# Kernel tuning notes

Hardware: AMD Instinct MI355X
Metric: run time of the kernel (lower is better)

The kernel has to match this reference:

```python
import jax, jax.numpy as jnp
import numpy as np

B, G, D, H, KD = 32, 512, 128, 4, 32  # batch, graph, embed_dim, n_heads, key_dim=embed//heads
NORM = 1.0 / np.sqrt(KD).astype(np.float32)  # MultiHeadCompat norm_factor = 1/sqrt(key_dim)


def _uniform(k, shape, fan):
    s = 1.0 / np.sqrt(fan).astype(np.float32)
    return jax.random.uniform(k, shape, jnp.float32, -s, s)


def setup_inputs() -> dict:
    key = jax.random.key(0)
    ks = jax.random.split(key, 16)
    inp = {
        "h": jax.random.normal(ks[0], (B, G, D), jnp.float32),
        "pos_pickup": jax.random.randint(ks[1], (B,), 0, G),
        "pos_delivery": jax.random.randint(ks[2], (B,), 0, G),
        "rec": jax.random.randint(ks[3], (B, G), 0, G),
        # compater_insert1 / compater_insert2 projections: (n_heads, input_dim, key_dim)
        "Wq1": _uniform(ks[4], (H, D, KD), KD),
        "Wk1": _uniform(ks[5], (H, D, KD), KD),
        "Wq2": _uniform(ks[6], (H, D, KD), KD),
        "Wk2": _uniform(ks[7], (H, D, KD), KD),
        # agg MLP(16, 32, 32, 1); stored as (in, out) so y = x @ W + b
        "fc1_w": _uniform(ks[8], (16, 32), 16),
        "fc1_b": _uniform(ks[9], (32,), 32),
        "fc2_w": _uniform(ks[10], (32, 32), 32),
        "fc2_b": _uniform(ks[11], (32,), 32),
        "fc3_w": _uniform(ks[12], (32, 1), 32),
        "fc3_b": _uniform(ks[13], (1,), 1),
    }
    return inp


def _compat(qv, hh, Wq, Wk):
    # qv: (B, D) single query node; hh: (B, G, D)
    Q = jnp.einsum('bd,hdk->bhk', qv, Wq)       # (B, H, K)
    K = jnp.einsum('bgd,hdk->bhgk', hh, Wk)     # (B, H, G, K)
    return NORM * jnp.einsum('bhk,bhgk->bgh', Q, K)  # (B, G, H)


def reference(h, pos_pickup, pos_delivery, rec, Wq1, Wk1, Wq2, Wk2,
              fc1_w, fc1_b, fc2_w, fc2_b, fc3_w, fc3_b):
    b, g, d = h.shape
    ar = jnp.arange(b)
    h_pickup = h[ar, pos_pickup]      # (B, D)
    h_delivery = h[ar, pos_delivery]  # (B, D)
    h_neighbour = jnp.take_along_axis(h, rec[:, :, None], axis=1)  # (B, G, D)

    shp = (b, g, g, 4)
    c_pp = jnp.broadcast_to(_compat(h_pickup, h, Wq1, Wk1)[:, :, None, :], shp)
    c_po = jnp.broadcast_to(_compat(h_pickup, h_neighbour, Wq2, Wk2)[:, :, None, :], shp)
    c_dp = jnp.broadcast_to(_compat(h_delivery, h, Wq1, Wk1)[:, None, :, :], shp)
    c_do = jnp.broadcast_to(_compat(h_delivery, h_neighbour, Wq2, Wk2)[:, None, :, :], shp)
    x = jnp.concatenate([c_pp, c_po, c_dp, c_do], axis=-1)  # (B, G, G, 16)

    # agg MLP (dropout p=0.05 is identity at inference)
    x = jax.nn.relu(x @ fc1_w + fc1_b)
    x = jax.nn.relu(x @ fc2_w + fc2_b)
    return (x @ fc3_w + fc3_b)[..., 0]  # (B, G, G)
```

## Files before the change

### kernel.cpp

```cpp
#include <hip/hip_runtime.h>


#define B 32
#define G 512
#define D 128
#define NH 4
#define KD 32
#define NORMF 0.17677669529663687f

#define WS_APQ 0
#define WS_APO 16384
#define WS_ADP 32768
#define WS_ADO 49152
#define WS_P   65536
#define WS_Q   589824

typedef float v16f __attribute__((ext_vector_type(16)));
typedef _Float16 v8h __attribute__((ext_vector_type(8)));
typedef __fp16 v2fp __attribute__((ext_vector_type(2)));

union H8 { v8h v; v2fp h2[4]; };

__global__ __launch_bounds__(128) void precompute_A(
    const float* __restrict__ h, const int* __restrict__ pp, const int* __restrict__ pd,
    const float* __restrict__ Wq1, const float* __restrict__ Wk1,
    const float* __restrict__ Wq2, const float* __restrict__ Wk2,
    float* __restrict__ ws) {
  const int b = blockIdx.x;
  const int t = threadIdx.x;
  __shared__ float hp[D], hd[D];
  __shared__ float q1p[NH * KD], q2p[NH * KD], q1d[NH * KD], q2d[NH * KD];

  hp[t] = h[(b * G + pp[b]) * D + t];
  hd[t] = h[(b * G + pd[b]) * D + t];
  __syncthreads();

  {
    const int hh = t >> 5, k = t & 31;
    const float* wq1 = Wq1 + hh * D * KD + k;
    const float* wq2 = Wq2 + hh * D * KD + k;
    float s1p = 0.f, s2p = 0.f, s1d = 0.f, s2d = 0.f;
    for (int d = 0; d < D; ++d) {
      const float w1 = wq1[d * KD], w2 = wq2[d * KD];
      const float xp = hp[d], xd = hd[d];
      s1p = fmaf(xp, w1, s1p);
      s2p = fmaf(xp, w2, s2p);
      s1d = fmaf(xd, w1, s1d);
      s2d = fmaf(xd, w2, s2d);
    }
    q1p[t] = s1p; q2p[t] = s2p; q1d[t] = s1d; q2d[t] = s2d;
  }
  __syncthreads();

  const int d = t;
  for (int hh = 0; hh < NH; ++hh) {
    const float* wk1 = Wk1 + hh * D * KD + d * KD;
    const float* wk2 = Wk2 + hh * D * KD + d * KD;
    float apq = 0.f, apo = 0.f, adp = 0.f, ado = 0.f;
#pragma unroll
    for (int k = 0; k < KD; ++k) {
      const float w1 = wk1[k], w2 = wk2[k];
      apq = fmaf(q1p[hh * 32 + k], w1, apq);
      adp = fmaf(q1d[hh * 32 + k], w1, adp);
      apo = fmaf(q2p[hh * 32 + k], w2, apo);
      ado = fmaf(q2d[hh * 32 + k], w2, ado);
    }
    const int o = b * (NH * D) + hh * D + d;
    ws[WS_APQ + o] = NORMF * apq;
    ws[WS_APO + o] = NORMF * apo;
    ws[WS_ADP + o] = NORMF * adp;
    ws[WS_ADO + o] = NORMF * ado;
  }
}

__global__ __launch_bounds__(256) void compute_PQ(
    const float* __restrict__ h, const int* __restrict__ rec,
    const float* __restrict__ fc1_w, const float* __restrict__ fc1_b,
    float* __restrict__ ws) {
  const int bx = blockIdx.x;
  const int b = bx >> 3, g0 = (bx & 7) * 64;
  const int t = threadIdx.x;
  const int gl = t & 63;
  const int hh = __builtin_amdgcn_readfirstlane(t >> 6);
  const int g = g0 + gl;

  __shared__ float sc[64][17];
  __shared__ float sout[64][33];

  const float* Apq = ws + WS_APQ + (b * NH + hh) * D;
  const float* Apo = ws + WS_APO + (b * NH + hh) * D;
  const float* Adp = ws + WS_ADP + (b * NH + hh) * D;
  const float* Ado = ws + WS_ADO + (b * NH + hh) * D;
  const float4* hg4 = (const float4*)(h + ((size_t)b * G + g) * D);
  const float4* hn4 = (const float4*)(h + ((size_t)b * G + rec[b * G + g]) * D);

  float cpp = 0.f, cpo = 0.f, cdp = 0.f, cdo = 0.f;
#pragma unroll 4
  for (int d4 = 0; d4 < 32; ++d4) {
    const float4 x = hg4[d4], y = hn4[d4];
    const float4 a1 = *(const float4*)(Apq + d4 * 4);
    const float4 a2 = *(const float4*)(Apo + d4 * 4);
    const float4 a3 = *(const float4*)(Adp + d4 * 4);
    const float4 a4 = *(const float4*)(Ado + d4 * 4);
    cpp = fmaf(x.x, a1.x, fmaf(x.y, a1.y, fmaf(x.z, a1.z, fmaf(x.w, a1.w, cpp))));
    cpo = fmaf(y.x, a2.x, fmaf(y.y, a2.y, fmaf(y.z, a2.z, fmaf(y.w, a2.w, cpo))));
    cdp = fmaf(x.x, a3.x, fmaf(x.y, a3.y, fmaf(x.z, a3.z, fmaf(x.w, a3.w, cdp))));
    cdo = fmaf(y.x, a4.x, fmaf(y.y, a4.y, fmaf(y.z, a4.z, fmaf(y.w, a4.w, cdo))));
  }
  sc[gl][hh] = cpp; sc[gl][4 + hh] = cpo; sc[gl][8 + hh] = cdp; sc[gl][12 + hh] = cdo;
  __syncthreads();

  float u[16];
#pragma unroll
  for (int i = 0; i < 16; ++i) u[i] = sc[gl][i];

  float pv[8], qv[8];
#pragma unroll
  for (int jj = 0; jj < 8; ++jj) {
    const int j = hh * 8 + jj;
    float p = 0.f, q = fc1_b[j];
#pragma unroll
    for (int i = 0; i < 8; ++i) {
      p = fmaf(u[i], fc1_w[i * 32 + j], p);
      q = fmaf(u[8 + i], fc1_w[(8 + i) * 32 + j], q);
    }
    pv[jj] = p; qv[jj] = q;
  }

#pragma unroll
  for (int jj = 0; jj < 8; ++jj) sout[gl][hh * 8 + jj] = pv[jj];
  __syncthreads();
  {
    float* dst = ws + WS_P + ((size_t)b * G + g0) * 32;
#pragma unroll
    for (int i = t; i < 2048; i += 256) dst[i] = sout[i >> 5][i & 31];
  }
  __syncthreads();
#pragma unroll
  for (int jj = 0; jj < 8; ++jj) sout[gl][hh * 8 + jj] = qv[jj];
  __syncthreads();
  {
    float* dst = ws + WS_Q + ((size_t)b * G + g0) * 32;
#pragma unroll
    for (int i = t; i < 2048; i += 256) dst[i] = sout[i >> 5][i & 31];
  }
}

__global__ __launch_bounds__(256) void mlp_pairs(
    const float* __restrict__ ws,
    const float* __restrict__ fc2_w, const float* __restrict__ fc2_b,
    const float* __restrict__ fc3_w, const float* __restrict__ fc3_b,
    float* __restrict__ out) {
  const int b = blockIdx.z;
  const int g1_0 = blockIdx.y * 16;
  const int g2_0 = blockIdx.x * 256;
  const int t = threadIdx.x;
  const int w = t >> 6, l = t & 63;
  const int col = l & 31;
  const int half = l >> 5;
  const int kb = half * 8;

  __shared__ float sP[16 * 32];
  {
    const float* Pg = ws + WS_P + ((size_t)b * G + g1_0) * 32;
    sP[t] = Pg[t];
    sP[t + 256] = Pg[t + 256];
  }

  v8h A0, A1;
#pragma unroll
  for (int j = 0; j < 8; ++j) {
    A0[j] = (_Float16)fc2_w[(kb + j) * 32 + col];
    A1[j] = (_Float16)fc2_w[(16 + kb + j) * 32 + col];
  }
  float biasv[16], w3v[16];
#pragma unroll
  for (int r = 0; r < 16; ++r) {
    const int n = (r & 3) + 8 * (r >> 2) + 4 * half;
    biasv[r] = fc2_b[n];
    w3v[r]   = fc3_w[n];
  }
  const float b3 = fc3_b[0];

  float4 q[2][4];
#pragma unroll
  for (int c = 0; c < 2; ++c) {
    const float* qp = ws + WS_Q +
        ((size_t)b * G + g2_0 + w * 64 + c * 32 + col) * 32;
    q[c][0] = *(const float4*)(qp + kb);
    q[c][1] = *(const float4*)(qp + kb + 4);
    q[c][2] = *(const float4*)(qp + 16 + kb);
    q[c][3] = *(const float4*)(qp + 16 + kb + 4);
  }
  __syncthreads();

  const size_t outbase = ((size_t)b * G + g1_0) * G + g2_0 + w * 64;
  for (int g1 = 0; g1 < 16; ++g1) {
    const float* pr = &sP[g1 * 32];
    const float4 p0 = *(const float4*)(pr + kb);
    const float4 p1 = *(const float4*)(pr + kb + 4);
    const float4 p2 = *(const float4*)(pr + 16 + kb);
    const float4 p3 = *(const float4*)(pr + 16 + kb + 4);

    float s[2];
#pragma unroll
    for (int c = 0; c < 2; ++c) {
      H8 B0, B1;
      B0.h2[0] = __builtin_amdgcn_cvt_pkrtz(fmaxf(p0.x + q[c][0].x, 0.f),
                                            fmaxf(p0.y + q[c][0].y, 0.f));
      B0.h2[1] = __builtin_amdgcn_cvt_pkrtz(fmaxf(p0.z + q[c][0].z, 0.f),
                                            fmaxf(p0.w + q[c][0].w, 0.f));
      B0.h2[2] = __builtin_amdgcn_cvt_pkrtz(fmaxf(p1.x + q[c][1].x, 0.f),
                                            fmaxf(p1.y + q[c][1].y, 0.f));
      B0.h2[3] = __builtin_amdgcn_cvt_pkrtz(fmaxf(p1.z + q[c][1].z, 0.f),
                                            fmaxf(p1.w + q[c][1].w, 0.f));
      B1.h2[0] = __builtin_amdgcn_cvt_pkrtz(fmaxf(p2.x + q[c][2].x, 0.f),
                                            fmaxf(p2.y + q[c][2].y, 0.f));
      B1.h2[1] = __builtin_amdgcn_cvt_pkrtz(fmaxf(p2.z + q[c][2].z, 0.f),
                                            fmaxf(p2.w + q[c][2].w, 0.f));
      B1.h2[2] = __builtin_amdgcn_cvt_pkrtz(fmaxf(p3.x + q[c][3].x, 0.f),
                                            fmaxf(p3.y + q[c][3].y, 0.f));
      B1.h2[3] = __builtin_amdgcn_cvt_pkrtz(fmaxf(p3.z + q[c][3].z, 0.f),
                                            fmaxf(p3.w + q[c][3].w, 0.f));

      v16f acc;
#pragma unroll
      for (int r = 0; r < 16; ++r) acc[r] = biasv[r];
      acc = __builtin_amdgcn_mfma_f32_32x32x16_f16(A0, B0.v, acc, 0, 0, 0);
      acc = __builtin_amdgcn_mfma_f32_32x32x16_f16(A1, B1.v, acc, 0, 0, 0);

      float sc = 0.f;
#pragma unroll
      for (int r = 0; r < 16; ++r)
        sc = fmaf(fmaxf(acc[r], 0.f), w3v[r], sc);
      s[c] = sc;
    }
    const float t0 = s[0] + __shfl_xor(s[0], 32);
    const float t1 = s[1] + __shfl_xor(s[1], 32);
    out[outbase + (size_t)g1 * G + l] = (l < 32 ? t0 : t1) + b3;
  }
}

extern "C" void kernel_launch(void* const* d_in, const int* in_sizes, int n_in,
                              void* d_out, int out_size, void* d_ws, size_t ws_size,
                              hipStream_t stream) {
  const float* h     = (const float*)d_in[0];
  const int*   pp    = (const int*)d_in[1];
  const int*   pd    = (const int*)d_in[2];
  const int*   rec   = (const int*)d_in[3];
  const float* Wq1   = (const float*)d_in[4];
  const float* Wk1   = (const float*)d_in[5];
  const float* Wq2   = (const float*)d_in[6];
  const float* Wk2   = (const float*)d_in[7];
  const float* fc1_w = (const float*)d_in[8];
  const float* fc1_b = (const float*)d_in[9];
  const float* fc2_w = (const float*)d_in[10];
  const float* fc2_b = (const float*)d_in[11];
  const float* fc3_w = (const float*)d_in[12];
  const float* fc3_b = (const float*)d_in[13];
  float* out = (float*)d_out;
  float* ws  = (float*)d_ws;

  precompute_A<<<dim3(B), dim3(128), 0, stream>>>(h, pp, pd, Wq1, Wk1, Wq2, Wk2, ws);
  compute_PQ<<<dim3(256), dim3(256), 0, stream>>>(h, rec, fc1_w, fc1_b, ws);
  mlp_pairs<<<dim3(2, 32, 32), dim3(256), 0, stream>>>(
      ws, fc2_w, fc2_b, fc3_w, fc3_b, out);
}
```

Before: 156.9 us.

## Store P/Q layer-1 partials in fp16 and build MFMA operands with packed half math

The precompute kernel now writes the per-node fc1 partial sums P and Q as packed fp16 instead of fp32. This halves workspace traffic and shared memory for P. The pair kernel forms the MFMA B operands with packed half add and max instead of per-element fp32 add, max and convert, and it splits the final dot product into two accumulators. The add and ReLU now run in fp16 rather than fp32, which costs some accuracy.

```diff
diff --git a/kernel.cpp b/kernel.cpp
--- a/kernel.cpp
+++ b/kernel.cpp
@@ -12,14 +12,18 @@
 #define WS_APO 16384
 #define WS_ADP 32768
 #define WS_ADO 49152
-#define WS_P   65536
-#define WS_Q   589824
+#define WS_P16H 131072
+#define WS_Q16H 655360
 
 typedef float v16f __attribute__((ext_vector_type(16)));
 typedef _Float16 v8h __attribute__((ext_vector_type(8)));
-typedef __fp16 v2fp __attribute__((ext_vector_type(2)));
-
-union H8 { v8h v; v2fp h2[4]; };
+typedef _Float16 h2 __attribute__((ext_vector_type(2)));
+
+union Q8 {
+  uint4 u;
+  h2 h[4];
+  v8h v;
+};
 
 __global__ __launch_bounds__(128) void precompute_A(
     const float* __restrict__ h, const int* __restrict__ pp, const int* __restrict__ pd,
@@ -131,18 +135,30 @@
   for (int jj = 0; jj < 8; ++jj) sout[gl][hh * 8 + jj] = pv[jj];
   __syncthreads();
   {
-    float* dst = ws + WS_P + ((size_t)b * G + g0) * 32;
-#pragma unroll
-    for (int i = t; i < 2048; i += 256) dst[i] = sout[i >> 5][i & 31];
+    unsigned* dst = (unsigned*)((unsigned short*)ws + WS_P16H) +
+                    ((size_t)b * G + g0) * 16;
+#pragma unroll
+    for (int i = t; i < 1024; i += 256) {
+      const int row = i >> 4, c0 = (2 * i) & 31;
+      __fp16 __attribute__((ext_vector_type(2))) pk =
+          __builtin_amdgcn_cvt_pkrtz(sout[row][c0], sout[row][c0 + 1]);
+      dst[i] = *(const unsigned*)&pk;
+    }
   }
   __syncthreads();
 #pragma unroll
   for (int jj = 0; jj < 8; ++jj) sout[gl][hh * 8 + jj] = qv[jj];
   __syncthreads();
   {
-    float* dst = ws + WS_Q + ((size_t)b * G + g0) * 32;
-#pragma unroll
-    for (int i = t; i < 2048; i += 256) dst[i] = sout[i >> 5][i & 31];
+    unsigned* dst = (unsigned*)((unsigned short*)ws + WS_Q16H) +
+                    ((size_t)b * G + g0) * 16;
+#pragma unroll
+    for (int i = t; i < 1024; i += 256) {
+      const int row = i >> 4, c0 = (2 * i) & 31;
+      __fp16 __attribute__((ext_vector_type(2))) pk =
+          __builtin_amdgcn_cvt_pkrtz(sout[row][c0], sout[row][c0 + 1]);
+      dst[i] = *(const unsigned*)&pk;
+    }
   }
 }
 
@@ -160,11 +176,11 @@
   const int half = l >> 5;
   const int kb = half * 8;
 
-  __shared__ float sP[16 * 32];
-  {
-    const float* Pg = ws + WS_P + ((size_t)b * G + g1_0) * 32;
-    sP[t] = Pg[t];
-    sP[t + 256] = Pg[t + 256];
+  __shared__ __align__(16) unsigned short sPh[16 * 32];
+  {
+    const unsigned* Psrc = (const unsigned*)((const unsigned short*)ws + WS_P16H) +
+                           ((size_t)b * G + g1_0) * 16;
+    ((unsigned*)sPh)[t] = Psrc[t];
   }
 
   v8h A0, A1;
@@ -173,67 +189,51 @@
     A0[j] = (_Float16)fc2_w[(kb + j) * 32 + col];
     A1[j] = (_Float16)fc2_w[(16 + kb + j) * 32 + col];
   }
-  float biasv[16], w3v[16];
+  v16f biasC;
+  float w3v[16];
 #pragma unroll
   for (int r = 0; r < 16; ++r) {
     const int n = (r & 3) + 8 * (r >> 2) + 4 * half;
-    biasv[r] = fc2_b[n];
+    biasC[r] = fc2_b[n];
     w3v[r]   = fc3_w[n];
   }
   const float b3 = fc3_b[0];
 
-  float4 q[2][4];
+  Q8 q0[2], q1[2];
 #pragma unroll
   for (int c = 0; c < 2; ++c) {
-    const float* qp = ws + WS_Q +
-        ((size_t)b * G + g2_0 + w * 64 + c * 32 + col) * 32;
-    q[c][0] = *(const float4*)(qp + kb);
-    q[c][1] = *(const float4*)(qp + kb + 4);
-    q[c][2] = *(const float4*)(qp + 16 + kb);
-    q[c][3] = *(const float4*)(qp + 16 + kb + 4);
-  }
-  __syncthreads();
-
+    const unsigned short* qp = (const unsigned short*)ws + WS_Q16H +
+        ((size_t)b * G + g2_0 + (2 * w + c) * 32 + col) * 32;
+    q0[c].u = *(const uint4*)(qp + kb);
+    q1[c].u = *(const uint4*)(qp + 16 + kb);
+  }
+  __syncthreads();
+
+  const h2 zero = {(_Float16)0.0f, (_Float16)0.0f};
   const size_t outbase = ((size_t)b * G + g1_0) * G + g2_0 + w * 64;
   for (int g1 = 0; g1 < 16; ++g1) {
-    const float* pr = &sP[g1 * 32];
-    const float4 p0 = *(const float4*)(pr + kb);
-    const float4 p1 = *(const float4*)(pr + kb + 4);
-    const float4 p2 = *(const float4*)(pr + 16 + kb);
-    const float4 p3 = *(const float4*)(pr + 16 + kb + 4);
+    const Q8 p0 = *(const Q8*)(sPh + g1 * 32 + kb);
+    const Q8 p1 = *(const Q8*)(sPh + g1 * 32 + 16 + kb);
 
     float s[2];
 #pragma unroll
     for (int c = 0; c < 2; ++c) {
-      H8 B0, B1;
-      B0.h2[0] = __builtin_amdgcn_cvt_pkrtz(fmaxf(p0.x + q[c][0].x, 0.f),
-                                            fmaxf(p0.y + q[c][0].y, 0.f));
-      B0.h2[1] = __builtin_amdgcn_cvt_pkrtz(fmaxf(p0.z + q[c][0].z, 0.f),
-                                            fmaxf(p0.w + q[c][0].w, 0.f));
-      B0.h2[2] = __builtin_amdgcn_cvt_pkrtz(fmaxf(p1.x + q[c][1].x, 0.f),
-                                            fmaxf(p1.y + q[c][1].y, 0.f));
-      B0.h2[3] = __builtin_amdgcn_cvt_pkrtz(fmaxf(p1.z + q[c][1].z, 0.f),
-                                            fmaxf(p1.w + q[c][1].w, 0.f));
-      B1.h2[0] = __builtin_amdgcn_cvt_pkrtz(fmaxf(p2.x + q[c][2].x, 0.f),
-                                            fmaxf(p2.y + q[c][2].y, 0.f));
-      B1.h2[1] = __builtin_amdgcn_cvt_pkrtz(fmaxf(p2.z + q[c][2].z, 0.f),
-                                            fmaxf(p2.w + q[c][2].w, 0.f));
-      B1.h2[2] = __builtin_amdgcn_cvt_pkrtz(fmaxf(p3.x + q[c][3].x, 0.f),
-                                            fmaxf(p3.y + q[c][3].y, 0.f));
-      B1.h2[3] = __builtin_amdgcn_cvt_pkrtz(fmaxf(p3.z + q[c][3].z, 0.f),
-                                            fmaxf(p3.w + q[c][3].w, 0.f));
-
-      v16f acc;
-#pragma unroll
-      for (int r = 0; r < 16; ++r) acc[r] = biasv[r];
-      acc = __builtin_amdgcn_mfma_f32_32x32x16_f16(A0, B0.v, acc, 0, 0, 0);
+      Q8 B0, B1;
+#pragma unroll
+      for (int i = 0; i < 4; ++i) {
+        B0.h[i] = __builtin_elementwise_max(p0.h[i] + q0[c].h[i], zero);
+        B1.h[i] = __builtin_elementwise_max(p1.h[i] + q1[c].h[i], zero);
+      }
+      v16f acc = __builtin_amdgcn_mfma_f32_32x32x16_f16(A0, B0.v, biasC, 0, 0, 0);
       acc = __builtin_amdgcn_mfma_f32_32x32x16_f16(A1, B1.v, acc, 0, 0, 0);
 
-      float sc = 0.f;
-#pragma unroll
-      for (int r = 0; r < 16; ++r)
-        sc = fmaf(fmaxf(acc[r], 0.f), w3v[r], sc);
-      s[c] = sc;
+      float e0 = 0.f, e1 = 0.f;
+#pragma unroll
+      for (int r = 0; r < 16; r += 2) {
+        e0 = fmaf(fmaxf(acc[r], 0.f), w3v[r], e0);
+        e1 = fmaf(fmaxf(acc[r + 1], 0.f), w3v[r + 1], e1);
+      }
+      s[c] = e0 + e1;
     }
     const float t0 = s[0] + __shfl_xor(s[0], 32);
     const float t1 = s[1] + __shfl_xor(s[1], 32);
```

After: 152.2 us. 3.0% less time.
